# Kernel tuning notes

Hardware: AMD Instinct MI355X
Metric: run time of the kernel (lower is better)

## Reference

```python
import jax, jax.numpy as jnp
import numpy as np

# Model dims
B = 64            # scenes (memory batch)
APER = 16         # agents per scene (uniform `length`)
A = B * APER      # total agents = sum(length)
TPAST = 20
TFUT = 30         # len_future
C = 256           # controller_size
M = 128           # memory_m
N = 256           # memory_n
H = 5             # num_heads (future modes)
SPACE = N // APER # per-agent write slot band
EMB = 16
D = C + M         # decoder hidden size


def _gru(x, h, wih, whh, bih, bhh):
    """torch.nn.GRU single-cell step."""
    gi = x @ wih.T + bih
    gh = h @ whh.T + bhh
    ir, iz, inn = jnp.split(gi, 3, axis=-1)
    hr, hz, hn = jnp.split(gh, 3, axis=-1)
    r = jax.nn.sigmoid(ir + hr)
    z = jax.nn.sigmoid(iz + hz)
    n = jnp.tanh(inn + r * hn)
    return (1.0 - z) * n + z * h


def _address(k, beta, mem, mask):
    """NTM content addressing: beta-sharpened masked softmax over cosine sims.
    k: (...,B,APER,M), beta: (...,B,APER,1), mem: (B,N,M), mask: (APER,N)."""
    kn = k / (jnp.linalg.norm(k, axis=-1, keepdims=True) + 1e-16)
    mn = mem / (jnp.linalg.norm(mem, axis=-1, keepdims=True) + 1e-16)
    sim = jnp.einsum('...bam,bnm->...ban', kn, mn)
    logits = beta * sim + (mask - 1.0) * 1e9
    return jax.nn.softmax(logits, axis=-1)


def setup_inputs() -> dict:
    key = jax.random.key(0)
    ks = iter(jax.random.split(key, 64))
    def nrm(shape, scale):
        return jax.random.normal(next(ks), shape, dtype=jnp.float32) * scale
    inp = dict(
        past=nrm((A, TPAST, 2), 1.0),
        past_rel=nrm((A, TPAST, 2), 1.0),
        ep_w1=nrm((8, 2), 0.7), ep_b1=jnp.zeros(8), ep_w2=nrm((EMB, 8), 0.35), ep_b2=jnp.zeros(EMB),
        er_w1=nrm((8, 2), 0.7), er_b1=jnp.zeros(8), er_w2=nrm((EMB, 8), 0.35), er_b2=jnp.zeros(EMB),
        enc_wih=nrm((3 * C, EMB + M), 1.0 / np.sqrt(EMB + M)), enc_whh=nrm((3 * C, C), 1.0 / np.sqrt(C)),
        enc_bih=jnp.zeros(3 * C), enc_bhh=jnp.zeros(3 * C),
        rel_wih=nrm((3 * C, EMB), 1.0 / np.sqrt(EMB)), rel_whh=nrm((3 * C, C), 1.0 / np.sqrt(C)),
        rel_bih=jnp.zeros(3 * C), rel_bhh=jnp.zeros(3 * C),
        dec_wih=nrm((3 * D, D), 1.0 / np.sqrt(D)), dec_whh=nrm((3 * D, D), 1.0 / np.sqrt(D)),
        dec_bih=jnp.zeros(3 * D), dec_bhh=jnp.zeros(3 * D),
        out_w=nrm((2, D), 1.0 / np.sqrt(D)), out_b=jnp.zeros(2),
        read_w=nrm((H, M + 1, C), 1.0 / np.sqrt(C)), read_b=jnp.zeros((H, M + 1)),
        write_w=nrm((3 * M + 1, C), 1.0 / np.sqrt(C)), write_b=jnp.zeros(3 * M + 1),
        init_r=nrm((1, M), 0.01),
        h_bias=nrm((1, C), 0.05), h_rel_bias=nrm((1, C), 0.05), h_fut_bias=nrm((1, D), 0.05),
        mem_bias=nrm((N, M), 0.05),
    )
    return inp


def reference(past, past_rel, ep_w1, ep_b1, ep_w2, ep_b2, er_w1, er_b1, er_w2, er_b2,
              enc_wih, enc_whh, enc_bih, enc_bhh, rel_wih, rel_whh, rel_bih, rel_bhh,
              dec_wih, dec_whh, dec_bih, dec_bhh, out_w, out_b,
              read_w, read_b, write_w, write_b,
              init_r, h_bias, h_rel_bias, h_fut_bias, mem_bias):
    # Per-agent disjoint write bands; read mask = other agents' bands.
    owner = jnp.arange(N) // SPACE
    mask_w = (owner[None, :] == jnp.arange(APER)[:, None]).astype(jnp.float32)  # (APER,N)
    mask_r = 1.0 - mask_w

    def mlp(x, w1, b1, w2, b2):
        return jax.nn.relu(x @ w1.T + b1) @ w2.T + b2

    emb_p = jnp.transpose(mlp(past, ep_w1, ep_b1, ep_w2, ep_b2), (1, 0, 2))      # (T,A,16)
    emb_r = jnp.transpose(mlp(past_rel, er_w1, er_b1, er_w2, er_b2), (1, 0, 2))  # (T,A,16)

    def step(carry, xs):
        emb, embr = xs
        mem, h, hr, hf, r = carry
        h = _gru(jnp.concatenate([emb, r], axis=-1), h, enc_wih, enc_whh, enc_bih, enc_bhh)
        hr = _gru(embr, hr, rel_wih, rel_whh, rel_bih, rel_bhh)
        # write head: k, beta, erase, add
        wp = h @ write_w.T + write_b
        kw = jnp.tanh(wp[:, :M]).reshape(B, APER, M)
        betaw = jax.nn.softplus(wp[:, M:M + 1]).reshape(B, APER, 1)
        er = jax.nn.sigmoid(wp[:, M + 1:2 * M + 1]).reshape(B, APER, M)
        ad = jnp.tanh(wp[:, 2 * M + 1:]).reshape(B, APER, M)
        ww = _address(kw, betaw, mem, mask_w)                                    # (B,APER,N)
        # erase/add; write bands are disjoint across agents so aggregation is exact
        mem = mem * (1.0 - jnp.einsum('ban,bam->bnm', ww, er)) + jnp.einsum('ban,bam->bnm', ww, ad)
        # per-head reads
        rp = jnp.einsum('ac,hkc->hak', hr, read_w) + read_b[:, None, :]          # (H,A,M+1)
        kr = jnp.tanh(rp[..., :M]).reshape(H, B, APER, M)
        betar = jax.nn.softplus(rp[..., M:]).reshape(H, B, APER, 1)
        wr = _address(kr, betar, mem, mask_r)                                    # (H,B,APER,N)
        reads = jnp.einsum('hban,bnm->hbam', wr, mem).reshape(H, A, M)
        r = reads[0]
        # per-mode decoder
        dec_in = jnp.concatenate([jnp.broadcast_to(h[None], (H, A, C)), reads], axis=-1).reshape(H * A, D)
        hf = _gru(dec_in, hf, dec_wih, dec_whh, dec_bih, dec_bhh)
        out = (hf @ out_w.T + out_b).reshape(H, A, 2)
        return (mem, h, hr, hf, r), out

    carry0 = (jnp.broadcast_to(mem_bias[None], (B, N, M)),
              jnp.broadcast_to(h_bias, (A, C)),
              jnp.broadcast_to(h_rel_bias, (A, C)),
              jnp.broadcast_to(h_fut_bias, (H * A, D)),
              jnp.broadcast_to(init_r, (A, M)))
    carry, _ = jax.lax.scan(step, carry0, (emb_p, emb_r))
    zf = jnp.zeros((TFUT, A, EMB), dtype=past.dtype)
    carry, outs = jax.lax.scan(step, carry, (zf, zf))                            # (TFUT,H,A,2)
    pred_rel = jnp.transpose(outs, (2, 1, 0, 3))                                 # (A,H,TFUT,2)
    pred = past[:, -1][:, None, None, :] + jnp.cumsum(pred_rel, axis=2)
    return pred, pred_rel
```

## Files before the change

### kernel.cpp

```cpp
#include <hip/hip_runtime.h>
#include <math.h>

#define B_    64
#define APER_ 16
#define A_    1024
#define TPAST_ 20
#define TFUT_  30
#define C_    256
#define M_    128
#define N_    256
#define H_    5
#define EMB_  16
#define D_    384
#define TTOT_ 50

typedef short bf16x8 __attribute__((ext_vector_type(8)));
typedef float f32x4 __attribute__((ext_vector_type(4)));

__device__ __forceinline__ float sigmoidf_(float x) { return 1.0f / (1.0f + expf(-x)); }
__device__ __forceinline__ float softplusf_(float x) { return (x > 20.0f) ? x : log1pf(expf(x)); }
__device__ __forceinline__ unsigned short f2bf(float f) {
    unsigned u = __float_as_uint(f);
    return (unsigned short)((u + 0x7FFFu + ((u >> 16) & 1u)) >> 16);
}
__device__ __forceinline__ float bf2f(short s) {
    return __uint_as_float(((unsigned)(unsigned short)s) << 16);
}

__global__ __launch_bounds__(256) void convert_w(const float* __restrict__ src, short* __restrict__ dst,
                                                 int srcRows, int srcK, int dstK, int total)
{
    const int idx = blockIdx.x * 256 + threadIdx.x;
    if (idx >= total) return;
    const int r = idx / dstK, k = idx % dstK;
    float v = (k < srcK && r < srcRows) ? src[(size_t)r * srcK + k] : 0.f;
    dst[idx] = (short)f2bf(v);
}

__global__ __launch_bounds__(64) void gru_mfma(
    const short* __restrict__ X1, int K1,
    const short* __restrict__ X2, int K2,
    const short* __restrict__ Wih, int Kpad,
    const float* __restrict__ bih,
    const short* __restrict__ Hb, const short* __restrict__ Whh,
    const float* __restrict__ bhh,
    const float* __restrict__ Hprev,
    float* __restrict__ Hnew, short* __restrict__ Hnewb,
    int G)
{
    const int lane = threadIdx.x;
    const int rowBase = blockIdx.x * 32;
    const int colBase = blockIdx.y * 32;
    const int l16 = lane & 15;
    const int kb8 = (lane >> 4) * 8;

    f32x4 gi[3][2][2], gh[3][2][2];
    const f32x4 z4 = {0.f, 0.f, 0.f, 0.f};
    #pragma unroll
    for (int g = 0; g < 3; ++g)
        #pragma unroll
        for (int i = 0; i < 2; ++i)
            #pragma unroll
            for (int j = 0; j < 2; ++j) { gi[g][i][j] = z4; gh[g][i][j] = z4; }

    for (int kc = 0; kc < Kpad; kc += 32) {
        bf16x8 afr[2];
        const int k8 = kc + kb8;
        #pragma unroll
        for (int i = 0; i < 2; ++i) {
            const int r = rowBase + i * 16 + l16;
            bf16x8 v = {0, 0, 0, 0, 0, 0, 0, 0};
            if (k8 < K1) {
                if (X1) v = *(const bf16x8*)(X1 + (size_t)(r & 1023) * K1 + k8);
            } else if (k8 < K1 + K2) {
                v = *(const bf16x8*)(X2 + (size_t)r * K2 + (k8 - K1));
            }
            afr[i] = v;
        }
        #pragma unroll
        for (int g = 0; g < 3; ++g)
            #pragma unroll
            for (int j = 0; j < 2; ++j) {
                const bf16x8 b = *(const bf16x8*)(Wih + (size_t)(g * G + colBase + j * 16 + l16) * Kpad + k8);
                gi[g][0][j] = __builtin_amdgcn_mfma_f32_16x16x32_bf16(afr[0], b, gi[g][0][j], 0, 0, 0);
                gi[g][1][j] = __builtin_amdgcn_mfma_f32_16x16x32_bf16(afr[1], b, gi[g][1][j], 0, 0, 0);
            }
    }
    for (int kc = 0; kc < G; kc += 32) {
        const int k8 = kc + kb8;
        bf16x8 afr[2];
        #pragma unroll
        for (int i = 0; i < 2; ++i)
            afr[i] = *(const bf16x8*)(Hb + (size_t)(rowBase + i * 16 + l16) * G + k8);
        #pragma unroll
        for (int g = 0; g < 3; ++g)
            #pragma unroll
            for (int j = 0; j < 2; ++j) {
                const bf16x8 b = *(const bf16x8*)(Whh + (size_t)(g * G + colBase + j * 16 + l16) * G + k8);
                gh[g][0][j] = __builtin_amdgcn_mfma_f32_16x16x32_bf16(afr[0], b, gh[g][0][j], 0, 0, 0);
                gh[g][1][j] = __builtin_amdgcn_mfma_f32_16x16x32_bf16(afr[1], b, gh[g][1][j], 0, 0, 0);
            }
    }

    const int r4 = (lane >> 4) * 4;
    #pragma unroll
    for (int j = 0; j < 2; ++j) {
        const int col = colBase + j * 16 + l16;
        const float bi0 = bih[col],         bh0 = bhh[col];
        const float bi1 = bih[G + col],     bh1 = bhh[G + col];
        const float bi2 = bih[2 * G + col], bh2 = bhh[2 * G + col];
        #pragma unroll
        for (int i = 0; i < 2; ++i) {
            #pragma unroll
            for (int q = 0; q < 4; ++q) {
                const int row = rowBase + i * 16 + r4 + q;
                const float rr = sigmoidf_(gi[0][i][j][q] + bi0 + gh[0][i][j][q] + bh0);
                const float zz = sigmoidf_(gi[1][i][j][q] + bi1 + gh[1][i][j][q] + bh1);
                const float nn = tanhf(gi[2][i][j][q] + bi2 + rr * (gh[2][i][j][q] + bh2));
                const float hp = Hprev[(size_t)row * G + col];
                const float hv = (1.f - zz) * nn + zz * hp;
                Hnew[(size_t)row * G + col] = hv;
                Hnewb[(size_t)row * G + col] = (short)f2bf(hv);
            }
        }
    }
}

__global__ __launch_bounds__(64) void gemm_mfma(
    const short* __restrict__ Xb, const short* __restrict__ Wb,
    const float* __restrict__ bias, float* __restrict__ Out,
    int Ncols, int K)
{
    const int lane = threadIdx.x;
    const int rowBase = blockIdx.x * 32;
    const int colBase = blockIdx.y * 32;
    const int l16 = lane & 15;
    const int kb8 = (lane >> 4) * 8;

    const f32x4 z4 = {0.f, 0.f, 0.f, 0.f};
    f32x4 acc[2][2] = {{z4, z4}, {z4, z4}};

    for (int kc = 0; kc < K; kc += 32) {
        const int k8 = kc + kb8;
        const bf16x8 a0 = *(const bf16x8*)(Xb + (size_t)(rowBase + l16) * K + k8);
        const bf16x8 a1 = *(const bf16x8*)(Xb + (size_t)(rowBase + 16 + l16) * K + k8);
        const bf16x8 b0 = *(const bf16x8*)(Wb + (size_t)(colBase + l16) * K + k8);
        const bf16x8 b1 = *(const bf16x8*)(Wb + (size_t)(colBase + 16 + l16) * K + k8);
        acc[0][0] = __builtin_amdgcn_mfma_f32_16x16x32_bf16(a0, b0, acc[0][0], 0, 0, 0);
        acc[0][1] = __builtin_amdgcn_mfma_f32_16x16x32_bf16(a0, b1, acc[0][1], 0, 0, 0);
        acc[1][0] = __builtin_amdgcn_mfma_f32_16x16x32_bf16(a1, b0, acc[1][0], 0, 0, 0);
        acc[1][1] = __builtin_amdgcn_mfma_f32_16x16x32_bf16(a1, b1, acc[1][1], 0, 0, 0);
    }
    const int r4 = (lane >> 4) * 4;
    #pragma unroll
    for (int j = 0; j < 2; ++j) {
        const int col = colBase + j * 16 + l16;
        if (col >= Ncols) continue;
        const float bv = bias[col];
        #pragma unroll
        for (int i = 0; i < 2; ++i)
            #pragma unroll
            for (int q = 0; q < 4; ++q) {
                const int row = rowBase + i * 16 + r4 + q;
                Out[(size_t)row * Ncols + col] = acc[i][j][q] + bv;
            }
    }
}

__global__ __launch_bounds__(256) void write_mem_k(const float* __restrict__ wp,
                                                   float* __restrict__ mem,
                                                   float* __restrict__ normsG)
{
    const int a = blockIdx.x;
    const int b = a >> 4, p = a & 15;
    __shared__ float kw[128], er[128], ad[128], red[256], ww[16], logit[16];
    __shared__ float buf[2048];
    __shared__ float beta_s, knorm_s;
    const int tid = threadIdx.x;
    const float* w = wp + (size_t)a * 385;
    if (tid < 128) {
        kw[tid] = tanhf(w[tid]);
        er[tid] = sigmoidf_(w[129 + tid]);
        ad[tid] = tanhf(w[257 + tid]);
    }
    if (tid == 0) beta_s = softplusf_(w[128]);
    __syncthreads();

    red[tid] = (tid < 128) ? kw[tid] * kw[tid] : 0.f;
    __syncthreads();
    for (int s = 128; s > 0; s >>= 1) { if (tid < s) red[tid] += red[tid + s]; __syncthreads(); }
    if (tid == 0) knorm_s = sqrtf(red[0]) + 1e-16f;
    __syncthreads();

    const int s = tid >> 4, j = tid & 15;
    float dot = 0.f, ss = 0.f;
    {
        const float* mrow = mem + ((size_t)(b * N_) + p * 16 + s) * M_;
        for (int k = j; k < 128; k += 16) { float v = mrow[k]; dot += kw[k] * v; ss += v * v; }
    }
    red[tid] = dot; __syncthreads();
    for (int st = 8; st > 0; st >>= 1) { if (j < st) red[tid] += red[tid + st]; __syncthreads(); }
    float dotf = red[s * 16];
    __syncthreads();
    red[tid] = ss; __syncthreads();
    for (int st = 8; st > 0; st >>= 1) { if (j < st) red[tid] += red[tid + st]; __syncthreads(); }
    float ssf = red[s * 16];
    if (j == 0) {
        float mn = sqrtf(ssf) + 1e-16f;
        logit[s] = beta_s * (dotf / (mn * knorm_s));
    }
    __syncthreads();
    if (tid == 0) {
        float mx = -1e30f;
        for (int i = 0; i < 16; ++i) mx = fmaxf(mx, logit[i]);
        float sum = 0.f;
        for (int i = 0; i < 16; ++i) { float e = __expf(logit[i] - mx); ww[i] = e; sum += e; }
        float inv = 1.f / sum;
        for (int i = 0; i < 16; ++i) ww[i] *= inv;
    }
    __syncthreads();
    for (int idx = tid; idx < 16 * 128; idx += 256) {
        int si = idx >> 7, m = idx & 127;
        size_t g = ((size_t)(b * N_) + p * 16 + si) * M_ + m;
        float wwv = ww[si];
        float v = mem[g] * (1.f - wwv * er[m]) + wwv * ad[m];
        mem[g] = v;
        buf[idx] = v;
    }
    __syncthreads();
    {
        float ssq = 0.f;
        #pragma unroll
        for (int i = 0; i < 8; ++i) { float v = buf[s * 128 + j + 16 * i]; ssq += v * v; }
        #pragma unroll
        for (int m = 1; m < 16; m <<= 1) ssq += __shfl_xor(ssq, m);
        if (j == 0) normsG[b * N_ + p * 16 + s] = sqrtf(ssq) + 1e-16f;
    }
}

__global__ __launch_bounds__(256) void read_k2(const float* __restrict__ rp,
                                               const float* __restrict__ mem,
                                               const float* __restrict__ normsG,
                                               short* __restrict__ reads_b)
{
    const int b = blockIdx.x;
    const int h = blockIdx.y;
    __shared__ __align__(16) float kq[16 * 132];
    __shared__ float S[16 * 260];
    __shared__ float beta_s[16], knorm_s[16], inv_s[16];
    const int t = threadIdx.x;
    const int a = t >> 4;
    const int sub = t & 15;

    {
        const float* base = rp + ((size_t)(b * 16 + a)) * 645 + h * 129;
        const int k0 = sub * 8;
        float v[8]; float ss = 0.f;
        #pragma unroll
        for (int r = 0; r < 8; ++r) { v[r] = tanhf(base[k0 + r]); ss += v[r] * v[r]; }
        float* dst = kq + a * 132 + k0;
        *(float4*)dst = make_float4(v[0], v[1], v[2], v[3]);
        *(float4*)(dst + 4) = make_float4(v[4], v[5], v[6], v[7]);
        #pragma unroll
        for (int m = 1; m < 16; m <<= 1) ss += __shfl_xor(ss, m);
        if (sub == 0) {
            knorm_s[a] = sqrtf(ss) + 1e-16f;
            beta_s[a] = softplusf_(base[128]);
        }
    }
    __syncthreads();

    {
        const int wave = t >> 6, lane = t & 63;
        const int l16 = lane & 15, kb8 = (lane >> 4) * 8;
        const int slotBase = wave * 64;
        const f32x4 z4 = {0.f, 0.f, 0.f, 0.f};
        f32x4 acc[4] = {z4, z4, z4, z4};
        const float* mb = mem + (size_t)b * N_ * M_;
        #pragma unroll
        for (int kc = 0; kc < 128; kc += 32) {
            const float* ap = kq + l16 * 132 + kc + kb8;
            bf16x8 ah, al;
            #pragma unroll
            for (int r = 0; r < 8; ++r) {
                const float av = ap[r];
                const short hv = (short)f2bf(av);
                ah[r] = hv; al[r] = (short)f2bf(av - bf2f(hv));
            }
            #pragma unroll
            for (int tt = 0; tt < 4; ++tt) {
                const float* bp = mb + (size_t)(slotBase + tt * 16 + l16) * M_ + kc + kb8;
                bf16x8 bh, bl;
                #pragma unroll
                for (int r = 0; r < 8; ++r) {
                    const float bv = bp[r];
                    const short hv = (short)f2bf(bv);
                    bh[r] = hv; bl[r] = (short)f2bf(bv - bf2f(hv));
                }
                acc[tt] = __builtin_amdgcn_mfma_f32_16x16x32_bf16(ah, bh, acc[tt], 0, 0, 0);
                acc[tt] = __builtin_amdgcn_mfma_f32_16x16x32_bf16(ah, bl, acc[tt], 0, 0, 0);
                acc[tt] = __builtin_amdgcn_mfma_f32_16x16x32_bf16(al, bh, acc[tt], 0, 0, 0);
            }
        }
        const int r4 = (lane >> 4) * 4;
        #pragma unroll
        for (int tt = 0; tt < 4; ++tt) {
            const int slot = slotBase + tt * 16 + l16;
            const float nv = normsG[b * N_ + slot];
            #pragma unroll
            for (int q = 0; q < 4; ++q) {
                const int aq = r4 + q;
                const float lg = ((slot >> 4) == aq) ? -1e30f
                               : beta_s[aq] * acc[tt][q] / (nv * knorm_s[aq]);
                S[aq * 260 + slot] = lg;
            }
        }
    }
    __syncthreads();

    {
        float mx = -1e30f;
        #pragma unroll
        for (int i = 0; i < 16; ++i) mx = fmaxf(mx, S[a * 260 + sub + 16 * i]);
        #pragma unroll
        for (int m = 1; m < 16; m <<= 1) mx = fmaxf(mx, __shfl_xor(mx, m));
        float e[16]; float sum = 0.f;
        #pragma unroll
        for (int i = 0; i < 16; ++i) { e[i] = __expf(S[a * 260 + sub + 16 * i] - mx); sum += e[i]; }
        #pragma unroll
        for (int i = 0; i < 16; ++i) S[a * 260 + sub + 16 * i] = e[i];
        #pragma unroll
        for (int m = 1; m < 16; m <<= 1) sum += __shfl_xor(sum, m);
        if (sub == 0) inv_s[a] = 1.f / sum;
    }
    __syncthreads();

    {
        const int m0 = sub * 8;
        const float* mb = mem + (size_t)b * N_ * M_ + m0;
        float acc[8];
        #pragma unroll
        for (int r = 0; r < 8; ++r) acc[r] = 0.f;
        const float* Sa = S + a * 260;
        #pragma unroll 4
        for (int n = 0; n < N_; ++n) {
            const float w = Sa[n];
            const float4 v0 = *(const float4*)(mb + (size_t)n * M_);
            const float4 v1 = *(const float4*)(mb + (size_t)n * M_ + 4);
            acc[0] = fmaf(w, v0.x, acc[0]); acc[1] = fmaf(w, v0.y, acc[1]);
            acc[2] = fmaf(w, v0.z, acc[2]); acc[3] = fmaf(w, v0.w, acc[3]);
            acc[4] = fmaf(w, v1.x, acc[4]); acc[5] = fmaf(w, v1.y, acc[5]);
            acc[6] = fmaf(w, v1.z, acc[6]); acc[7] = fmaf(w, v1.w, acc[7]);
        }
        const float inv = inv_s[a];
        short pk[8];
        #pragma unroll
        for (int r = 0; r < 8; ++r) pk[r] = (short)f2bf(acc[r] * inv);
        *(bf16x8*)(reads_b + ((size_t)h * A_ + b * 16 + a) * M_ + m0) = *(bf16x8*)pk;
    }
}

__global__ __launch_bounds__(256) void out_k(const float* __restrict__ hf,
                                             const float* __restrict__ out_w,
                                             const float* __restrict__ out_b,
                                             float* __restrict__ predrel, int t)
{
    const int row = blockIdx.x * 4 + (threadIdx.x >> 6);
    const int lane = threadIdx.x & 63;
    const float* hrow = hf + (size_t)row * D_;
    float a0 = 0.f, a1 = 0.f;
    for (int k = lane; k < D_; k += 64) {
        float v = hrow[k];
        a0 += v * out_w[k];
        a1 += v * out_w[D_ + k];
    }
    for (int off = 32; off > 0; off >>= 1) { a0 += __shfl_down(a0, off); a1 += __shfl_down(a1, off); }
    if (lane == 0) {
        int hh = row >> 10;
        int a = row & 1023;
        float* o = predrel + (((size_t)a * H_ + hh) * TFUT_ + t) * 2;
        o[0] = a0 + out_b[0];
        o[1] = a1 + out_b[1];
    }
}

__global__ __launch_bounds__(256) void cumsum_k(const float* __restrict__ past,
                                                const float* __restrict__ predrel,
                                                float* __restrict__ pred)
{
    const int idx = blockIdx.x * 256 + threadIdx.x;
    if (idx >= A_ * H_ * 2) return;
    const int c = idx & 1;
    const int ah = idx >> 1;
    const int a = ah / H_;
    float acc = past[((size_t)a * TPAST_ + TPAST_ - 1) * 2 + c];
    const float* pr = predrel + (size_t)ah * TFUT_ * 2 + c;
    float* pd = pred + (size_t)ah * TFUT_ * 2 + c;
    for (int t = 0; t < TFUT_; ++t) { acc += pr[t * 2]; pd[t * 2] = acc; }
}

__global__ __launch_bounds__(256) void embed_k(const float* __restrict__ x,
                                               const float* __restrict__ w1, const float* __restrict__ b1,
                                               const float* __restrict__ w2, const float* __restrict__ b2,
                                               short* __restrict__ emb)
{
    const int idx = blockIdx.x * 256 + threadIdx.x;
    if (idx >= A_ * TPAST_) return;
    const int a = idx / TPAST_, t = idx % TPAST_;
    const float x0 = x[(size_t)idx * 2], x1 = x[(size_t)idx * 2 + 1];
    float hbuf[8];
    #pragma unroll
    for (int j = 0; j < 8; ++j) hbuf[j] = fmaxf(0.f, w1[j * 2] * x0 + w1[j * 2 + 1] * x1 + b1[j]);
    short* e = emb + ((size_t)t * A_ + a) * EMB_;
    #pragma unroll
    for (int i = 0; i < 16; ++i) {
        float acc = b2[i];
        #pragma unroll
        for (int j = 0; j < 8; ++j) acc += w2[i * 8 + j] * hbuf[j];
        e[i] = (short)f2bf(acc);
    }
}

__global__ __launch_bounds__(256) void init_k(float* __restrict__ h, const float* __restrict__ h_bias, short* __restrict__ hb,
                                              float* __restrict__ hr, const float* __restrict__ hr_bias, short* __restrict__ hrb,
                                              float* __restrict__ hf, const float* __restrict__ hf_bias, short* __restrict__ hfb,
                                              short* __restrict__ reads_b, const float* __restrict__ init_r,
                                              float* __restrict__ mem,
                                              float* __restrict__ normsG, const float* __restrict__ mem_bias)
{
    const int idx = blockIdx.x * 256 + threadIdx.x;
    if (idx < B_ * N_ * M_) mem[idx] = mem_bias[idx & (N_ * M_ - 1)];
    if (idx < B_ * N_) {
        const float* r = mem_bias + (size_t)(idx & (N_ - 1)) * M_;
        float ss = 0.f;
        for (int k = 0; k < M_; ++k) ss += r[k] * r[k];
        normsG[idx] = sqrtf(ss) + 1e-16f;
    }
    if (idx < A_ * C_) {
        float v = h_bias[idx & (C_ - 1)];
        h[idx] = v; hb[idx] = (short)f2bf(v);
        v = hr_bias[idx & (C_ - 1)];
        hr[idx] = v; hrb[idx] = (short)f2bf(v);
    }
    if (idx < H_ * A_ * D_) {
        float v = hf_bias[idx % D_];
        hf[idx] = v; hfb[idx] = (short)f2bf(v);
    }
    if (idx < A_ * M_) reads_b[idx] = (short)f2bf(init_r[idx & (M_ - 1)]);
}

extern "C" void kernel_launch(void* const* d_in, const int* in_sizes, int n_in,
                              void* d_out, int out_size, void* d_ws, size_t ws_size,
                              hipStream_t stream)
{
    const float* past       = (const float*)d_in[0];
    const float* past_rel   = (const float*)d_in[1];
    const float* ep_w1      = (const float*)d_in[2];
    const float* ep_b1      = (const float*)d_in[3];
    const float* ep_w2      = (const float*)d_in[4];
    const float* ep_b2      = (const float*)d_in[5];
    const float* er_w1      = (const float*)d_in[6];
    const float* er_b1      = (const float*)d_in[7];
    const float* er_w2      = (const float*)d_in[8];
    const float* er_b2      = (const float*)d_in[9];
    const float* enc_wih    = (const float*)d_in[10];
    const float* enc_whh    = (const float*)d_in[11];
    const float* enc_bih    = (const float*)d_in[12];
    const float* enc_bhh    = (const float*)d_in[13];
    const float* rel_wih    = (const float*)d_in[14];
    const float* rel_whh    = (const float*)d_in[15];
    const float* rel_bih    = (const float*)d_in[16];
    const float* rel_bhh    = (const float*)d_in[17];
    const float* dec_wih    = (const float*)d_in[18];
    const float* dec_whh    = (const float*)d_in[19];
    const float* dec_bih    = (const float*)d_in[20];
    const float* dec_bhh    = (const float*)d_in[21];
    const float* out_w      = (const float*)d_in[22];
    const float* out_b      = (const float*)d_in[23];
    const float* read_w     = (const float*)d_in[24];
    const float* read_b     = (const float*)d_in[25];
    const float* write_w    = (const float*)d_in[26];
    const float* write_b    = (const float*)d_in[27];
    const float* init_r     = (const float*)d_in[28];
    const float* h_bias     = (const float*)d_in[29];
    const float* h_rel_bias = (const float*)d_in[30];
    const float* h_fut_bias = (const float*)d_in[31];
    const float* mem_bias   = (const float*)d_in[32];

    float* pred    = (float*)d_out;
    float* predrel = pred + (size_t)A_ * H_ * TFUT_ * 2;

    float* ws = (float*)d_ws;
    size_t off = 0;
    auto alloc = [&](size_t n) { float* p = ws + off; off += n; return p; };
    float* h0     = alloc((size_t)A_ * C_);
    float* h1     = alloc((size_t)A_ * C_);
    float* hr0    = alloc((size_t)A_ * C_);
    float* hr1    = alloc((size_t)A_ * C_);
    float* hf0    = alloc((size_t)H_ * A_ * D_);
    float* hf1    = alloc((size_t)H_ * A_ * D_);
    float* mem    = alloc((size_t)B_ * N_ * M_);
    float* wp     = alloc((size_t)A_ * 385);
    float* rp     = alloc((size_t)A_ * 645);
    float* normsG = alloc((size_t)B_ * N_);

    short* sws = (short*)(ws + off);
    size_t soff = 0;
    auto salloc = [&](size_t n) { short* p = sws + soff; soff += n; return p; };
    short* emb_p_b   = salloc((size_t)TPAST_ * A_ * EMB_);
    short* emb_r_b   = salloc((size_t)TPAST_ * A_ * EMB_);
    short* hb0       = salloc((size_t)A_ * C_);
    short* hb1       = salloc((size_t)A_ * C_);
    short* hrb0      = salloc((size_t)A_ * C_);
    short* hrb1      = salloc((size_t)A_ * C_);
    short* hfb0      = salloc((size_t)H_ * A_ * D_);
    short* hfb1      = salloc((size_t)H_ * A_ * D_);
    short* reads_b   = salloc((size_t)H_ * A_ * M_);
    short* enc_wih_b = salloc((size_t)768 * 160);
    short* enc_whh_b = salloc((size_t)768 * 256);
    short* rel_wih_b = salloc((size_t)768 * 32);
    short* rel_whh_b = salloc((size_t)768 * 256);
    short* dec_wih_b = salloc((size_t)1152 * 384);
    short* dec_whh_b = salloc((size_t)1152 * 384);
    short* write_w_b = salloc((size_t)416 * 256);
    short* read_w_b  = salloc((size_t)672 * 256);
    (void)ws_size; (void)in_sizes; (void)n_in; (void)out_size;

    auto cvt = [&](const float* s, short* d, int sr, int sk, int dr, int dk) {
        int total = dr * dk;
        convert_w<<<(total + 255) / 256, 256, 0, stream>>>(s, d, sr, sk, dk, total);
    };
    cvt(enc_wih, enc_wih_b, 768, 144, 768, 160);
    cvt(enc_whh, enc_whh_b, 768, 256, 768, 256);
    cvt(rel_wih, rel_wih_b, 768, 16, 768, 32);
    cvt(rel_whh, rel_whh_b, 768, 256, 768, 256);
    cvt(dec_wih, dec_wih_b, 1152, 384, 1152, 384);
    cvt(dec_whh, dec_whh_b, 1152, 384, 1152, 384);
    cvt(write_w, write_w_b, 385, 256, 416, 256);
    cvt(read_w, read_w_b, 645, 256, 672, 256);

    init_k<<<(B_ * N_ * M_ + 255) / 256, 256, 0, stream>>>(
        h0, h_bias, hb0, hr0, h_rel_bias, hrb0, hf0, h_fut_bias, hfb0,
        reads_b, init_r, mem, normsG, mem_bias);
    embed_k<<<(A_ * TPAST_ + 255) / 256, 256, 0, stream>>>(past, ep_w1, ep_b1, ep_w2, ep_b2, emb_p_b);
    embed_k<<<(A_ * TPAST_ + 255) / 256, 256, 0, stream>>>(past_rel, er_w1, er_b1, er_w2, er_b2, emb_r_b);

    float *hc = h0, *hn = h1, *hrc = hr0, *hrn = hr1, *hfc = hf0, *hfn = hf1;
    short *hbc = hb0, *hbn = hb1, *hrbc = hrb0, *hrbn = hrb1, *hfbc = hfb0, *hfbn = hfb1;

    const dim3 g_enc(A_ / 32, C_ / 32);
    const dim3 g_dec((H_ * A_) / 32, D_ / 32);
    const dim3 g_wp(A_ / 32, 13);
    const dim3 g_rp(A_ / 32, 21);
    const dim3 g_read(B_, H_);

    for (int t = 0; t < TTOT_; ++t) {
        const short* ep = (t < TPAST_) ? emb_p_b + (size_t)t * A_ * EMB_ : nullptr;
        const short* er = (t < TPAST_) ? emb_r_b + (size_t)t * A_ * EMB_ : nullptr;

        gru_mfma<<<g_enc, 64, 0, stream>>>(ep, 16, reads_b, 128,
                                           enc_wih_b, 160, enc_bih,
                                           hbc, enc_whh_b, enc_bhh,
                                           hc, hn, hbn, C_);
        gru_mfma<<<g_enc, 64, 0, stream>>>(er, 16, nullptr, 0,
                                           rel_wih_b, 32, rel_bih,
                                           hrbc, rel_whh_b, rel_bhh,
                                           hrc, hrn, hrbn, C_);
        gemm_mfma<<<g_wp, 64, 0, stream>>>(hbn, write_w_b, write_b, wp, 385, C_);
        write_mem_k<<<A_, 256, 0, stream>>>(wp, mem, normsG);
        gemm_mfma<<<g_rp, 64, 0, stream>>>(hrbn, read_w_b, read_b, rp, 645, C_);
        read_k2<<<g_read, 256, 0, stream>>>(rp, mem, normsG, reads_b);
        gru_mfma<<<g_dec, 64, 0, stream>>>(hbn, 256, reads_b, 128,
                                           dec_wih_b, 384, dec_bih,
                                           hfbc, dec_whh_b, dec_bhh,
                                           hfc, hfn, hfbn, D_);
        if (t >= TPAST_)
            out_k<<<(H_ * A_) / 4, 256, 0, stream>>>(hfn, out_w, out_b, predrel, t - TPAST_);

        float* tf;
        short* ts;
        tf = hc; hc = hn; hn = tf;      ts = hbc; hbc = hbn; hbn = ts;
        tf = hrc; hrc = hrn; hrn = tf;  ts = hrbc; hrbc = hrbn; hrbn = ts;
        tf = hfc; hfc = hfn; hfn = tf;  ts = hfbc; hfbc = hfbn; hfbn = ts;
    }
    cumsum_k<<<(A_ * H_ * 2 + 255) / 256, 256, 0, stream>>>(past, predrel, pred);
}
```

Measured before the change: 7.182 ms.

## Skew decoder GRU by one step and fuse per-step kernels into three phases

Restructures the time loop so the decoder GRU for step t-1 runs in the same launch as the encoder and relation GRUs for step t. It fuses the write and read projection GEMMs into the memory write and read kernels, and folds the output projection into the write phase. This cuts per-step kernel launches from up to eight to three and removes the wp/rp global round-trips. The cost is a more intricate skewed schedule with an extra tail launch, and the projections now use scalar FMA dot products instead of MFMA.

After: 10.42 ms. 1.45x slower.

```diff
diff --git a/kernel.cpp b/kernel.cpp
--- a/kernel.cpp
+++ b/kernel.cpp
@@ -27,17 +27,84 @@
     return __uint_as_float(((unsigned)(unsigned short)s) << 16);
 }
 
-__global__ __launch_bounds__(256) void convert_w(const float* __restrict__ src, short* __restrict__ dst,
-                                                 int srcRows, int srcK, int dstK, int total)
+struct Cvt { const float* src; short* dst; int rows, sk, dk, total; };
+struct Cvt8 { Cvt c[8]; };
+
+__global__ __launch_bounds__(256) void convert_all(Cvt8 p)
+{
+    const int stride = gridDim.x * 256;
+    #pragma unroll
+    for (int s = 0; s < 8; ++s) {
+        const Cvt d = p.c[s];
+        for (int idx = blockIdx.x * 256 + threadIdx.x; idx < d.total; idx += stride) {
+            const int r = idx / d.dk, k = idx % d.dk;
+            float v = (k < d.sk && r < d.rows) ? d.src[(size_t)r * d.sk + k] : 0.f;
+            d.dst[idx] = (short)f2bf(v);
+        }
+    }
+}
+
+__global__ __launch_bounds__(256) void embed2_k(const float* __restrict__ past, const float* __restrict__ past_rel,
+                                                const float* __restrict__ pw1, const float* __restrict__ pb1,
+                                                const float* __restrict__ pw2, const float* __restrict__ pb2,
+                                                const float* __restrict__ rw1, const float* __restrict__ rb1,
+                                                const float* __restrict__ rw2, const float* __restrict__ rb2,
+                                                short* __restrict__ emb_p, short* __restrict__ emb_r)
+{
+    const int idx0 = blockIdx.x * 256 + threadIdx.x;
+    const int half = A_ * TPAST_;
+    if (idx0 >= 2 * half) return;
+    const bool second = idx0 >= half;
+    const int idx = second ? idx0 - half : idx0;
+    const float* x = second ? past_rel : past;
+    const float* w1 = second ? rw1 : pw1; const float* b1 = second ? rb1 : pb1;
+    const float* w2 = second ? rw2 : pw2; const float* b2 = second ? rb2 : pb2;
+    short* emb = second ? emb_r : emb_p;
+
+    const int a = idx / TPAST_, t = idx % TPAST_;
+    const float x0 = x[(size_t)idx * 2], x1 = x[(size_t)idx * 2 + 1];
+    float hbuf[8];
+    #pragma unroll
+    for (int j = 0; j < 8; ++j) hbuf[j] = fmaxf(0.f, w1[j * 2] * x0 + w1[j * 2 + 1] * x1 + b1[j]);
+    short* e = emb + ((size_t)t * A_ + a) * EMB_;
+    #pragma unroll
+    for (int i = 0; i < 16; ++i) {
+        float acc = b2[i];
+        #pragma unroll
+        for (int j = 0; j < 8; ++j) acc += w2[i * 8 + j] * hbuf[j];
+        e[i] = (short)f2bf(acc);
+    }
+}
+
+__global__ __launch_bounds__(256) void init_k(float* __restrict__ h, const float* __restrict__ h_bias, short* __restrict__ hb,
+                                              float* __restrict__ hr, const float* __restrict__ hr_bias, short* __restrict__ hrb,
+                                              float* __restrict__ hf, const float* __restrict__ hf_bias, short* __restrict__ hfb,
+                                              short* __restrict__ reads_b, const float* __restrict__ init_r,
+                                              float* __restrict__ mem,
+                                              float* __restrict__ normsG, const float* __restrict__ mem_bias)
 {
     const int idx = blockIdx.x * 256 + threadIdx.x;
-    if (idx >= total) return;
-    const int r = idx / dstK, k = idx % dstK;
-    float v = (k < srcK && r < srcRows) ? src[(size_t)r * srcK + k] : 0.f;
-    dst[idx] = (short)f2bf(v);
-}
-
-__global__ __launch_bounds__(64) void gru_mfma(
+    if (idx < B_ * N_ * M_) mem[idx] = mem_bias[idx & (N_ * M_ - 1)];
+    if (idx < B_ * N_) {
+        const float* r = mem_bias + (size_t)(idx & (N_ - 1)) * M_;
+        float ss = 0.f;
+        for (int k = 0; k < M_; ++k) ss += r[k] * r[k];
+        normsG[idx] = sqrtf(ss) + 1e-16f;
+    }
+    if (idx < A_ * C_) {
+        float v = h_bias[idx & (C_ - 1)];
+        h[idx] = v; hb[idx] = (short)f2bf(v);
+        v = hr_bias[idx & (C_ - 1)];
+        hr[idx] = v; hrb[idx] = (short)f2bf(v);
+    }
+    if (idx < H_ * A_ * D_) {
+        float v = hf_bias[idx % D_];
+        hf[idx] = v; hfb[idx] = (short)f2bf(v);
+    }
+    if (idx < A_ * M_) reads_b[idx] = (short)f2bf(init_r[idx & (M_ - 1)]);
+}
+
+__device__ __forceinline__ void gru_tile(
     const short* __restrict__ X1, int K1,
     const short* __restrict__ X2, int K2,
     const short* __restrict__ Wih, int Kpad,
@@ -46,11 +113,8 @@
     const float* __restrict__ bhh,
     const float* __restrict__ Hprev,
     float* __restrict__ Hnew, short* __restrict__ Hnewb,
-    int G)
-{
-    const int lane = threadIdx.x;
-    const int rowBase = blockIdx.x * 32;
-    const int colBase = blockIdx.y * 32;
+    int G, int rowBase, int colBase, int lane)
+{
     const int l16 = lane & 15;
     const int kb8 = (lane >> 4) * 8;
 
@@ -126,64 +190,107 @@
     }
 }
 
-__global__ __launch_bounds__(64) void gemm_mfma(
-    const short* __restrict__ Xb, const short* __restrict__ Wb,
-    const float* __restrict__ bias, float* __restrict__ Out,
-    int Ncols, int K)
-{
-    const int lane = threadIdx.x;
-    const int rowBase = blockIdx.x * 32;
-    const int colBase = blockIdx.y * 32;
-    const int l16 = lane & 15;
-    const int kb8 = (lane >> 4) * 8;
-
-    const f32x4 z4 = {0.f, 0.f, 0.f, 0.f};
-    f32x4 acc[2][2] = {{z4, z4}, {z4, z4}};
-
-    for (int kc = 0; kc < K; kc += 32) {
-        const int k8 = kc + kb8;
-        const bf16x8 a0 = *(const bf16x8*)(Xb + (size_t)(rowBase + l16) * K + k8);
-        const bf16x8 a1 = *(const bf16x8*)(Xb + (size_t)(rowBase + 16 + l16) * K + k8);
-        const bf16x8 b0 = *(const bf16x8*)(Wb + (size_t)(colBase + l16) * K + k8);
-        const bf16x8 b1 = *(const bf16x8*)(Wb + (size_t)(colBase + 16 + l16) * K + k8);
-        acc[0][0] = __builtin_amdgcn_mfma_f32_16x16x32_bf16(a0, b0, acc[0][0], 0, 0, 0);
-        acc[0][1] = __builtin_amdgcn_mfma_f32_16x16x32_bf16(a0, b1, acc[0][1], 0, 0, 0);
-        acc[1][0] = __builtin_amdgcn_mfma_f32_16x16x32_bf16(a1, b0, acc[1][0], 0, 0, 0);
-        acc[1][1] = __builtin_amdgcn_mfma_f32_16x16x32_bf16(a1, b1, acc[1][1], 0, 0, 0);
-    }
-    const int r4 = (lane >> 4) * 4;
-    #pragma unroll
-    for (int j = 0; j < 2; ++j) {
-        const int col = colBase + j * 16 + l16;
-        if (col >= Ncols) continue;
-        const float bv = bias[col];
-        #pragma unroll
-        for (int i = 0; i < 2; ++i)
-            #pragma unroll
-            for (int q = 0; q < 4; ++q) {
-                const int row = rowBase + i * 16 + r4 + q;
-                Out[(size_t)row * Ncols + col] = acc[i][j][q] + bv;
-            }
-    }
-}
-
-__global__ __launch_bounds__(256) void write_mem_k(const float* __restrict__ wp,
-                                                   float* __restrict__ mem,
-                                                   float* __restrict__ normsG)
-{
-    const int a = blockIdx.x;
-    const int b = a >> 4, p = a & 15;
+__global__ __launch_bounds__(256) void phaseA(
+    const short* __restrict__ ep, const short* __restrict__ er,
+    const short* __restrict__ enc_wih, const float* __restrict__ enc_bih,
+    const short* __restrict__ enc_whh, const float* __restrict__ enc_bhh,
+    const short* __restrict__ rel_wih, const float* __restrict__ rel_bih,
+    const short* __restrict__ rel_whh, const float* __restrict__ rel_bhh,
+    const short* __restrict__ dec_wih, const float* __restrict__ dec_bih,
+    const short* __restrict__ dec_whh, const float* __restrict__ dec_bhh,
+    const float* __restrict__ hc, const short* __restrict__ hbc,
+    float* __restrict__ hn, short* __restrict__ hbn,
+    const float* __restrict__ hrc, const short* __restrict__ hrbc,
+    float* __restrict__ hrn, short* __restrict__ hrbn,
+    const float* __restrict__ hfc, const short* __restrict__ hfbc,
+    float* __restrict__ hfn, short* __restrict__ hfbn,
+    const short* __restrict__ reads_b,
+    int encBlocks, int relBlocks)
+{
+    const int bid = blockIdx.x;
+    const int wave = threadIdx.x >> 6;
+    const int lane = threadIdx.x & 63;
+
+    if (bid < encBlocks) {
+        const int tile = bid * 4 + wave;
+        gru_tile(ep, 16, reads_b, 128, enc_wih, 160, enc_bih,
+                 hbc, enc_whh, enc_bhh, hc, hn, hbn, C_,
+                 (tile >> 3) * 32, (tile & 7) * 32, lane);
+    } else if (bid < encBlocks + relBlocks) {
+        const int tile = (bid - encBlocks) * 4 + wave;
+        gru_tile(er, 16, nullptr, 0, rel_wih, 32, rel_bih,
+                 hrbc, rel_whh, rel_bhh, hrc, hrn, hrbn, C_,
+                 (tile >> 3) * 32, (tile & 7) * 32, lane);
+    } else {
+        const int tile = (bid - encBlocks - relBlocks) * 4 + wave;
+        gru_tile(hbc, 256, reads_b, 128, dec_wih, 384, dec_bih,
+                 hfbc, dec_whh, dec_bhh, hfc, hfn, hfbn, D_,
+                 (tile / 12) * 32, (tile % 12) * 32, lane);
+    }
+}
+
+__global__ __launch_bounds__(256) void phaseB(
+    const short* __restrict__ hbn, const short* __restrict__ write_w_b,
+    const float* __restrict__ write_b,
+    float* __restrict__ mem, float* __restrict__ normsG,
+    const float* __restrict__ hfn, const float* __restrict__ out_w,
+    const float* __restrict__ out_b, float* __restrict__ predrel,
+    int outT, int agentBlocks)
+{
+    __shared__ float wl[388];
+    __shared__ __align__(16) short xs[256];
     __shared__ float kw[128], er[128], ad[128], red[256], ww[16], logit[16];
     __shared__ float buf[2048];
     __shared__ float beta_s, knorm_s;
     const int tid = threadIdx.x;
-    const float* w = wp + (size_t)a * 385;
+
+    if ((int)blockIdx.x >= agentBlocks) {
+        const int widx = ((int)blockIdx.x - agentBlocks) * 4 + (tid >> 6);
+        const int lane = tid & 63;
+        const int g = lane >> 3, li = lane & 7;
+        const int row = widx * 8 + g;
+        const float* hrow = hfn + (size_t)row * D_;
+        float a0 = 0.f, a1 = 0.f;
+        for (int k = li; k < D_; k += 8) {
+            const float v = hrow[k];
+            a0 += v * out_w[k];
+            a1 += v * out_w[D_ + k];
+        }
+        a0 += __shfl_xor(a0, 1); a0 += __shfl_xor(a0, 2); a0 += __shfl_xor(a0, 4);
+        a1 += __shfl_xor(a1, 1); a1 += __shfl_xor(a1, 2); a1 += __shfl_xor(a1, 4);
+        if (li == 0) {
+            const int hh = row >> 10, aa = row & 1023;
+            float* o = predrel + (((size_t)aa * H_ + hh) * TFUT_ + outT) * 2;
+            o[0] = a0 + out_b[0];
+            o[1] = a1 + out_b[1];
+        }
+        return;
+    }
+
+    const int a = blockIdx.x;
+    const int b = a >> 4, p = a & 15;
+
+    if (tid < 32) ((bf16x8*)xs)[tid] = ((const bf16x8*)(hbn + (size_t)a * C_))[tid];
+    __syncthreads();
+    for (int c = tid; c < 385; c += 256) {
+        const short* wr = write_w_b + (size_t)c * 256;
+        float acc = write_b[c];
+        for (int k = 0; k < 256; k += 8) {
+            const bf16x8 wv = *(const bf16x8*)(wr + k);
+            const bf16x8 xv = *(const bf16x8*)(xs + k);
+            #pragma unroll
+            for (int r = 0; r < 8; ++r) acc = fmaf(bf2f(xv[r]), bf2f(wv[r]), acc);
+        }
+        wl[c] = acc;
+    }
+    __syncthreads();
+
     if (tid < 128) {
-        kw[tid] = tanhf(w[tid]);
-        er[tid] = sigmoidf_(w[129 + tid]);
-        ad[tid] = tanhf(w[257 + tid]);
-    }
-    if (tid == 0) beta_s = softplusf_(w[128]);
+        kw[tid] = tanhf(wl[tid]);
+        er[tid] = sigmoidf_(wl[129 + tid]);
+        ad[tid] = tanhf(wl[257 + tid]);
+    }
+    if (tid == 0) beta_s = softplusf_(wl[128]);
     __syncthreads();
 
     red[tid] = (tid < 128) ? kw[tid] * kw[tid] : 0.f;
@@ -238,40 +345,56 @@
     }
 }
 
-__global__ __launch_bounds__(256) void read_k2(const float* __restrict__ rp,
-                                               const float* __restrict__ mem,
-                                               const float* __restrict__ normsG,
-                                               short* __restrict__ reads_b)
-{
-    const int b = blockIdx.x;
-    const int h = blockIdx.y;
+__global__ __launch_bounds__(256) void phaseC(
+    const short* __restrict__ hrbn, const short* __restrict__ read_w_b,
+    const float* __restrict__ read_b,
+    const float* __restrict__ mem, const float* __restrict__ normsG,
+    short* __restrict__ reads_b)
+{
+    const int task = blockIdx.x;
+    const int h = task >> 6, b = task & 63;
+    __shared__ __align__(16) short xs[16 * 256];
     __shared__ __align__(16) float kq[16 * 132];
     __shared__ float S[16 * 260];
     __shared__ float beta_s[16], knorm_s[16], inv_s[16];
-    const int t = threadIdx.x;
-    const int a = t >> 4;
-    const int sub = t & 15;
+    const int tid = threadIdx.x;
 
     {
-        const float* base = rp + ((size_t)(b * 16 + a)) * 645 + h * 129;
-        const int k0 = sub * 8;
-        float v[8]; float ss = 0.f;
-        #pragma unroll
-        for (int r = 0; r < 8; ++r) { v[r] = tanhf(base[k0 + r]); ss += v[r] * v[r]; }
-        float* dst = kq + a * 132 + k0;
-        *(float4*)dst = make_float4(v[0], v[1], v[2], v[3]);
-        *(float4*)(dst + 4) = make_float4(v[4], v[5], v[6], v[7]);
-        #pragma unroll
-        for (int m = 1; m < 16; m <<= 1) ss += __shfl_xor(ss, m);
-        if (sub == 0) {
-            knorm_s[a] = sqrtf(ss) + 1e-16f;
-            beta_s[a] = softplusf_(base[128]);
-        }
+        const bf16x8* src = (const bf16x8*)(hrbn + (size_t)(b * 16) * C_);
+        ((bf16x8*)xs)[tid] = src[tid];
+        ((bf16x8*)xs)[tid + 256] = src[tid + 256];
+    }
+    __syncthreads();
+
+    for (int o = tid; o < 16 * 129; o += 256) {
+        const int a = o / 129, c = o % 129;
+        const short* wr = read_w_b + (size_t)(h * 129 + c) * 256;
+        const short* xr = xs + a * 256;
+        float acc = read_b[h * 129 + c];
+        for (int k = 0; k < 256; k += 8) {
+            const bf16x8 wv = *(const bf16x8*)(wr + k);
+            const bf16x8 xv = *(const bf16x8*)(xr + k);
+            #pragma unroll
+            for (int r = 0; r < 8; ++r) acc = fmaf(bf2f(xv[r]), bf2f(wv[r]), acc);
+        }
+        if (c < 128) kq[a * 132 + c] = tanhf(acc);
+        else beta_s[a] = softplusf_(acc);
     }
     __syncthreads();
 
     {
-        const int wave = t >> 6, lane = t & 63;
+        const int a = tid >> 4, sub = tid & 15;
+        float ssk = 0.f;
+        #pragma unroll
+        for (int i = 0; i < 8; ++i) { const float v = kq[a * 132 + sub + 16 * i]; ssk += v * v; }
+        #pragma unroll
+        for (int m = 1; m < 16; m <<= 1) ssk += __shfl_xor(ssk, m);
+        if (sub == 0) knorm_s[a] = sqrtf(ssk) + 1e-16f;
+    }
+    __syncthreads();
+
+    {
+        const int wave = tid >> 6, lane = tid & 63;
         const int l16 = lane & 15, kb8 = (lane >> 4) * 8;
         const int slotBase = wave * 64;
         const f32x4 z4 = {0.f, 0.f, 0.f, 0.f};
@@ -319,6 +442,7 @@
     __syncthreads();
 
     {
+        const int a = tid >> 4, sub = tid & 15;
         float mx = -1e30f;
         #pragma unroll
         for (int i = 0; i < 16; ++i) mx = fmaxf(mx, S[a * 260 + sub + 16 * i]);
@@ -336,6 +460,7 @@
     __syncthreads();
 
     {
+        const int a = tid >> 4, sub = tid & 15;
         const int m0 = sub * 8;
         const float* mb = mem + (size_t)b * N_ * M_ + m0;
         float acc[8];
@@ -360,30 +485,6 @@
     }
 }
 
-__global__ __launch_bounds__(256) void out_k(const float* __restrict__ hf,
-                                             const float* __restrict__ out_w,
-                                             const float* __restrict__ out_b,
-                                             float* __restrict__ predrel, int t)
-{
-    const int row = blockIdx.x * 4 + (threadIdx.x >> 6);
-    const int lane = threadIdx.x & 63;
-    const float* hrow = hf + (size_t)row * D_;
-    float a0 = 0.f, a1 = 0.f;
-    for (int k = lane; k < D_; k += 64) {
-        float v = hrow[k];
-        a0 += v * out_w[k];
-        a1 += v * out_w[D_ + k];
-    }
-    for (int off = 32; off > 0; off >>= 1) { a0 += __shfl_down(a0, off); a1 += __shfl_down(a1, off); }
-    if (lane == 0) {
-        int hh = row >> 10;
-        int a = row & 1023;
-        float* o = predrel + (((size_t)a * H_ + hh) * TFUT_ + t) * 2;
-        o[0] = a0 + out_b[0];
-        o[1] = a1 + out_b[1];
-    }
-}
-
 __global__ __launch_bounds__(256) void cumsum_k(const float* __restrict__ past,
                                                 const float* __restrict__ predrel,
                                                 float* __restrict__ pred)
@@ -397,56 +498,6 @@
     const float* pr = predrel + (size_t)ah * TFUT_ * 2 + c;
     float* pd = pred + (size_t)ah * TFUT_ * 2 + c;
     for (int t = 0; t < TFUT_; ++t) { acc += pr[t * 2]; pd[t * 2] = acc; }
-}
-
-__global__ __launch_bounds__(256) void embed_k(const float* __restrict__ x,
-                                               const float* __restrict__ w1, const float* __restrict__ b1,
-                                               const float* __restrict__ w2, const float* __restrict__ b2,
-                                               short* __restrict__ emb)
-{
-    const int idx = blockIdx.x * 256 + threadIdx.x;
-    if (idx >= A_ * TPAST_) return;
-    const int a = idx / TPAST_, t = idx % TPAST_;
-    const float x0 = x[(size_t)idx * 2], x1 = x[(size_t)idx * 2 + 1];
-    float hbuf[8];
-    #pragma unroll
-    for (int j = 0; j < 8; ++j) hbuf[j] = fmaxf(0.f, w1[j * 2] * x0 + w1[j * 2 + 1] * x1 + b1[j]);
-    short* e = emb + ((size_t)t * A_ + a) * EMB_;
-    #pragma unroll
-    for (int i = 0; i < 16; ++i) {
-        float acc = b2[i];
-        #pragma unroll
-        for (int j = 0; j < 8; ++j) acc += w2[i * 8 + j] * hbuf[j];
-        e[i] = (short)f2bf(acc);
-    }
-}
-
-__global__ __launch_bounds__(256) void init_k(float* __restrict__ h, const float* __restrict__ h_bias, short* __restrict__ hb,
-                                              float* __restrict__ hr, const float* __restrict__ hr_bias, short* __restrict__ hrb,
-                                              float* __restrict__ hf, const float* __restrict__ hf_bias, short* __restrict__ hfb,
-                                              short* __restrict__ reads_b, const float* __restrict__ init_r,
-                                              float* __restrict__ mem,
-                                              float* __restrict__ normsG, const float* __restrict__ mem_bias)
-{
-    const int idx = blockIdx.x * 256 + threadIdx.x;
-    if (idx < B_ * N_ * M_) mem[idx] = mem_bias[idx & (N_ * M_ - 1)];
-    if (idx < B_ * N_) {
-        const float* r = mem_bias + (size_t)(idx & (N_ - 1)) * M_;
-        float ss = 0.f;
-        for (int k = 0; k < M_; ++k) ss += r[k] * r[k];
-        normsG[idx] = sqrtf(ss) + 1e-16f;
-    }
-    if (idx < A_ * C_) {
-        float v = h_bias[idx & (C_ - 1)];
-        h[idx] = v; hb[idx] = (short)f2bf(v);
-        v = hr_bias[idx & (C_ - 1)];
-        hr[idx] = v; hrb[idx] = (short)f2bf(v);
-    }
-    if (idx < H_ * A_ * D_) {
-        float v = hf_bias[idx % D_];
-        hf[idx] = v; hfb[idx] = (short)f2bf(v);
-    }
-    if (idx < A_ * M_) reads_b[idx] = (short)f2bf(init_r[idx & (M_ - 1)]);
 }
 
 extern "C" void kernel_launch(void* const* d_in, const int* in_sizes, int n_in,
@@ -500,8 +551,6 @@
     float* hf0    = alloc((size_t)H_ * A_ * D_);
     float* hf1    = alloc((size_t)H_ * A_ * D_);
     float* mem    = alloc((size_t)B_ * N_ * M_);
-    float* wp     = alloc((size_t)A_ * 385);
-    float* rp     = alloc((size_t)A_ * 645);
     float* normsG = alloc((size_t)B_ * N_);
 
     short* sws = (short*)(ws + off);
@@ -522,66 +571,72 @@
     short* rel_whh_b = salloc((size_t)768 * 256);
     short* dec_wih_b = salloc((size_t)1152 * 384);
     short* dec_whh_b = salloc((size_t)1152 * 384);
-    short* write_w_b = salloc((size_t)416 * 256);
-    short* read_w_b  = salloc((size_t)672 * 256);
+    short* write_w_b = salloc((size_t)385 * 256);
+    short* read_w_b  = salloc((size_t)645 * 256);
     (void)ws_size; (void)in_sizes; (void)n_in; (void)out_size;
 
-    auto cvt = [&](const float* s, short* d, int sr, int sk, int dr, int dk) {
-        int total = dr * dk;
-        convert_w<<<(total + 255) / 256, 256, 0, stream>>>(s, d, sr, sk, dk, total);
-    };
-    cvt(enc_wih, enc_wih_b, 768, 144, 768, 160);
-    cvt(enc_whh, enc_whh_b, 768, 256, 768, 256);
-    cvt(rel_wih, rel_wih_b, 768, 16, 768, 32);
-    cvt(rel_whh, rel_whh_b, 768, 256, 768, 256);
-    cvt(dec_wih, dec_wih_b, 1152, 384, 1152, 384);
-    cvt(dec_whh, dec_whh_b, 1152, 384, 1152, 384);
-    cvt(write_w, write_w_b, 385, 256, 416, 256);
-    cvt(read_w, read_w_b, 645, 256, 672, 256);
+    Cvt8 cp;
+    cp.c[0] = {enc_wih, enc_wih_b, 768, 144, 160, 768 * 160};
+    cp.c[1] = {enc_whh, enc_whh_b, 768, 256, 256, 768 * 256};
+    cp.c[2] = {rel_wih, rel_wih_b, 768, 16, 32, 768 * 32};
+    cp.c[3] = {rel_whh, rel_whh_b, 768, 256, 256, 768 * 256};
+    cp.c[4] = {dec_wih, dec_wih_b, 1152, 384, 384, 1152 * 384};
+    cp.c[5] = {dec_whh, dec_whh_b, 1152, 384, 384, 1152 * 384};
+    cp.c[6] = {write_w, write_w_b, 385, 256, 256, 385 * 256};
+    cp.c[7] = {read_w, read_w_b, 645, 256, 256, 645 * 256};
+    convert_all<<<1024, 256, 0, stream>>>(cp);
 
     init_k<<<(B_ * N_ * M_ + 255) / 256, 256, 0, stream>>>(
         h0, h_bias, hb0, hr0, h_rel_bias, hrb0, hf0, h_fut_bias, hfb0,
         reads_b, init_r, mem, normsG, mem_bias);
-    embed_k<<<(A_ * TPAST_ + 255) / 256, 256, 0, stream>>>(past, ep_w1, ep_b1, ep_w2, ep_b2, emb_p_b);
-    embed_k<<<(A_ * TPAST_ + 255) / 256, 256, 0, stream>>>(past_rel, er_w1, er_b1, er_w2, er_b2, emb_r_b);
+    embed2_k<<<(2 * A_ * TPAST_ + 255) / 256, 256, 0, stream>>>(
+        past, past_rel, ep_w1, ep_b1, ep_w2, ep_b2, er_w1, er_b1, er_w2, er_b2,
+        emb_p_b, emb_r_b);
 
     float *hc = h0, *hn = h1, *hrc = hr0, *hrn = hr1, *hfc = hf0, *hfn = hf1;
     short *hbc = hb0, *hbn = hb1, *hrbc = hrb0, *hrbn = hrb1, *hfbc = hfb0, *hfbn = hfb1;
-
-    const dim3 g_enc(A_ / 32, C_ / 32);
-    const dim3 g_dec((H_ * A_) / 32, D_ / 32);
-    const dim3 g_wp(A_ / 32, 13);
-    const dim3 g_rp(A_ / 32, 21);
-    const dim3 g_read(B_, H_);
 
     for (int t = 0; t < TTOT_; ++t) {
         const short* ep = (t < TPAST_) ? emb_p_b + (size_t)t * A_ * EMB_ : nullptr;
         const short* er = (t < TPAST_) ? emb_r_b + (size_t)t * A_ * EMB_ : nullptr;
 
-        gru_mfma<<<g_enc, 64, 0, stream>>>(ep, 16, reads_b, 128,
-                                           enc_wih_b, 160, enc_bih,
-                                           hbc, enc_whh_b, enc_bhh,
-                                           hc, hn, hbn, C_);
-        gru_mfma<<<g_enc, 64, 0, stream>>>(er, 16, nullptr, 0,
-                                           rel_wih_b, 32, rel_bih,
-                                           hrbc, rel_whh_b, rel_bhh,
-                                           hrc, hrn, hrbn, C_);
-        gemm_mfma<<<g_wp, 64, 0, stream>>>(hbn, write_w_b, write_b, wp, 385, C_);
-        write_mem_k<<<A_, 256, 0, stream>>>(wp, mem, normsG);
-        gemm_mfma<<<g_rp, 64, 0, stream>>>(hrbn, read_w_b, read_b, rp, 645, C_);
-        read_k2<<<g_read, 256, 0, stream>>>(rp, mem, normsG, reads_b);
-        gru_mfma<<<g_dec, 64, 0, stream>>>(hbn, 256, reads_b, 128,
-                                           dec_wih_b, 384, dec_bih,
-                                           hfbc, dec_whh_b, dec_bhh,
-                                           hfc, hfn, hfbn, D_);
-        if (t >= TPAST_)
-            out_k<<<(H_ * A_) / 4, 256, 0, stream>>>(hfn, out_w, out_b, predrel, t - TPAST_);
-
-        float* tf;
-        short* ts;
-        tf = hc; hc = hn; hn = tf;      ts = hbc; hbc = hbn; hbn = ts;
-        tf = hrc; hrc = hrn; hrn = tf;  ts = hrbc; hrbc = hrbn; hrbn = ts;
-        tf = hfc; hfc = hfn; hfn = tf;  ts = hfbc; hfbc = hfbn; hfbn = ts;
-    }
+        const int gridA = (t == 0) ? 128 : 608;
+        phaseA<<<gridA, 256, 0, stream>>>(
+            ep, er,
+            enc_wih_b, enc_bih, enc_whh_b, enc_bhh,
+            rel_wih_b, rel_bih, rel_whh_b, rel_bhh,
+            dec_wih_b, dec_bih, dec_whh_b, dec_bhh,
+            hc, hbc, hn, hbn,
+            hrc, hrbc, hrn, hrbn,
+            hfc, hfbc, hfn, hfbn,
+            reads_b, 64, 64);
+
+        const int gridB = (t >= 21) ? 1184 : 1024;
+        phaseB<<<gridB, 256, 0, stream>>>(
+            hbn, write_w_b, write_b, mem, normsG,
+            hfn, out_w, out_b, predrel, t - 21, 1024);
+
+        phaseC<<<320, 256, 0, stream>>>(hrbn, read_w_b, read_b, mem, normsG, reads_b);
+
+        float* tf; short* ts;
+        tf = hc; hc = hn; hn = tf;       ts = hbc; hbc = hbn; hbn = ts;
+        tf = hrc; hrc = hrn; hrn = tf;   ts = hrbc; hrbc = hrbn; hrbn = ts;
+        if (t >= 1) {
+            tf = hfc; hfc = hfn; hfn = tf;  ts = hfbc; hfbc = hfbn; hfbn = ts;
+        }
+    }
+
+    phaseA<<<480, 256, 0, stream>>>(
+        nullptr, nullptr,
+        enc_wih_b, enc_bih, enc_whh_b, enc_bhh,
+        rel_wih_b, rel_bih, rel_whh_b, rel_bhh,
+        dec_wih_b, dec_bih, dec_whh_b, dec_bhh,
+        hc, hbc, hn, hbn,
+        hrc, hrbc, hrn, hrbn,
+        hfc, hfbc, hfn, hfbn,
+        reads_b, 0, 0);
+    phaseB<<<160, 256, 0, stream>>>(
+        hbn, write_w_b, write_b, mem, normsG,
+        hfn, out_w, out_b, predrel, TFUT_ - 1, 0);
     cumsum_k<<<(A_ * H_ * 2 + 255) / 256, 256, 0, stream>>>(past, predrel, pred);
 }
```
